# Performance work log

Measured on AMD Instinct MI355X. Metric: run time of the kernel, lower is better.

## Reference

```python
import jax, jax.numpy as jnp
import numpy as np

SCALE_BASE = 512.0
GAMMA = 0.96875


def _rotate_every_two(x):
    x1 = x[..., ::2]
    x2 = x[..., 1::2]
    return jnp.stack([-x2, x1], axis=-1).reshape(x.shape)


def _dup_interleave(m):
    # [L, d/2] -> [L, d], each column duplicated: (a,b) -> (a,a,b,b)
    return jnp.repeat(m, 2, axis=-1)


def _xpos(x, downscale=False):
    # x: [B, L, d]; offset = 0 (parallel form)
    B, L, d = x.shape
    half = d // 2
    pos = jnp.arange(L, dtype=x.dtype)
    # xpos per-channel scale base
    sv = (jnp.arange(0, d, 2, dtype=x.dtype) + 0.4 * d) / (1.4 * d)   # [d/2]
    scale = sv[None, :] ** (pos[:, None] / SCALE_BASE)                 # [L, d/2]
    if downscale:
        scale = 1.0 / scale
    inv_freq = 1.0 / (10000.0 ** (jnp.arange(half, dtype=x.dtype) / half))
    sinusoid = pos[:, None] * inv_freq[None, :]                        # [L, d/2]
    sin = _dup_interleave(jnp.sin(sinusoid) * scale)                   # [L, d]
    cos = _dup_interleave(jnp.cos(sinusoid) * scale)                   # [L, d]
    return x * cos[None] + _rotate_every_two(x) * sin[None]


def _get_D(seq_len, dtype):
    idx = jnp.arange(seq_len)
    diff = idx[:, None] - idx[None, :]                                 # n - m
    safe = jnp.where(diff >= 0, diff, 0).astype(dtype)
    return jnp.where(diff >= 0, GAMMA ** safe, jnp.zeros((), dtype))   # [L, L]


def setup_inputs() -> dict:
    key = jax.random.key(0)
    k1, k2, k3, k4 = jax.random.split(key, 4)
    B, L, H, D = 2, 4096, 1024, 64
    X = jax.random.normal(k1, (B, L, H), dtype=jnp.float32)
    W_Q = jax.random.normal(k2, (H, D), dtype=jnp.float32) / H
    W_K = jax.random.normal(k3, (H, D), dtype=jnp.float32) / H
    W_V = jax.random.normal(k4, (H, D), dtype=jnp.float32) / H
    return {"X": X, "W_Q": W_Q, "W_K": W_K, "W_V": W_V}


def reference(X, W_Q, W_K, W_V):
    L = X.shape[1]
    Dmask = _get_D(L, X.dtype)                     # [L, L]
    Q = _xpos(X @ W_Q)                             # [B, L, d]
    K = _xpos(X @ W_K, downscale=True)             # [B, L, d]
    V = X @ W_V                                    # [B, L, v]
    ret = jnp.einsum('bnd,bmd->bnm', Q, K) * Dmask[None]  # [B, L, L]
    return ret @ V                                 # [B, L, v]
```

## Files before the change

### kernel.cpp

```cpp
#include <hip/hip_runtime.h>
#include <math.h>

#define NB 2
#define LL 4096
#define HH 1024
#define DD 64
#define CHK 64
#define NCH 64
#define BLROWS (NB*LL)
#define NCHT (NB*NCH)
#define GAMMA 0.96875f

typedef _Float16 f16x8 __attribute__((ext_vector_type(8)));
typedef _Float16 f16x4 __attribute__((ext_vector_type(4)));
typedef float    f32x4 __attribute__((ext_vector_type(4)));

#define WCH 12288

__global__ __launch_bounds__(256) void prep_w(
    const float* __restrict__ WQ, const float* __restrict__ WK,
    const float* __restrict__ WV, _Float16* __restrict__ Whg,
    _Float16* __restrict__ Wlg)
{
    const unsigned t = blockIdx.x * 256 + threadIdx.x;
    const unsigned kchunk = t / 1536u;
    const unsigned s = t - kchunk * 1536u;
    const int ct2  = s >> 6;
    const int lane = s & 63;
    const int n16  = ct2 >> 1;
    const int kt   = ct2 & 1;
    const int quad = lane >> 4;
    const int n    = n16 * 16 + (lane & 15);
    const int k0   = (int)kchunk * 64 + kt * 32 + quad * 8;
    const int m    = n >> 6;
    const int d    = n & 63;
    const float* Wm = (m == 0) ? WQ : (m == 1) ? WK : WV;
    f16x8 hv, lv;
#pragma unroll
    for (int j = 0; j < 8; ++j) {
        const float x = Wm[(size_t)(k0 + j) * DD + d] * 1024.f;
        const _Float16 h = (_Float16)x;
        hv[j] = h;
        lv[j] = (_Float16)(x - (float)h);
    }
    *(f16x8*)&Whg[(size_t)t * 8] = hv;
    *(f16x8*)&Wlg[(size_t)t * 8] = lv;
}

__global__ __launch_bounds__(256) void proj_mfma(
    const float* __restrict__ X, const _Float16* __restrict__ Whg,
    const _Float16* __restrict__ Wlg, _Float16* __restrict__ Qr,
    _Float16* __restrict__ Kr, _Float16* __restrict__ Vr)
{
    const int tid  = threadIdx.x;
    const int wv   = tid >> 6;
    const int lane = tid & 63;
    const int quad = lane >> 4;
    const int l15  = lane & 15;
    const int r0   = blockIdx.x * 32;

    f32x4 acc[6];
#pragma unroll
    for (int i = 0; i < 6; ++i) acc[i] = (f32x4){0.f, 0.f, 0.f, 0.f};

    for (int ch = 0; ch < 16; ++ch) {
        f16x8 ah[2][2], al[2][2];
#pragma unroll
        for (int rt = 0; rt < 2; ++rt) {
#pragma unroll
            for (int kt = 0; kt < 2; ++kt) {
                const float* xp = &X[(size_t)(r0 + rt * 16 + l15) * HH +
                                     ch * 64 + kt * 32 + quad * 8];
                const float4 xa = *(const float4*)&xp[0];
                const float4 xb = *(const float4*)&xp[4];
                const float xv[8] = {xa.x, xa.y, xa.z, xa.w,
                                     xb.x, xb.y, xb.z, xb.w};
                f16x8 hv, lv;
#pragma unroll
                for (int e = 0; e < 8; ++e) {
                    const _Float16 h = (_Float16)xv[e];
                    hv[e] = h;
                    lv[e] = (_Float16)(xv[e] - (float)h);
                }
                ah[rt][kt] = hv;
                al[rt][kt] = lv;
            }
        }
#pragma unroll
        for (int kt = 0; kt < 2; ++kt) {
#pragma unroll
            for (int cj = 0; cj < 3; ++cj) {
                const int ctg = wv * 3 + cj;
                const size_t off = (size_t)ch * WCH +
                                   (size_t)(((ctg * 2 + kt) * 64 + lane)) * 8;
                const f16x8 bh = *(const f16x8*)&Whg[off];
                const f16x8 bl = *(const f16x8*)&Wlg[off];
#pragma unroll
                for (int rt = 0; rt < 2; ++rt) {
                    acc[rt * 3 + cj] = __builtin_amdgcn_mfma_f32_16x16x32_f16(
                        ah[rt][kt], bh, acc[rt * 3 + cj], 0, 0, 0);
                    acc[rt * 3 + cj] = __builtin_amdgcn_mfma_f32_16x16x32_f16(
                        ah[rt][kt], bl, acc[rt * 3 + cj], 0, 0, 0);
                    acc[rt * 3 + cj] = __builtin_amdgcn_mfma_f32_16x16x32_f16(
                        al[rt][kt], bh, acc[rt * 3 + cj], 0, 0, 0);
                }
            }
        }
    }

    const int c16 = l15;
#pragma unroll
    for (int rt = 0; rt < 2; ++rt) {
#pragma unroll
        for (int cj = 0; cj < 3; ++cj) {
            const int ctg = wv * 3 + cj;
            const f32x4 v = acc[rt * 3 + cj];
            const int col = ctg * 16 + c16;
            const int mat = ctg >> 2;
            const int d   = col & 63;
            if (mat < 2) {
                const int i2 = d >> 1;
                const float sv   = (2.f * (float)i2 + 25.6f) / 89.6f;
                const float l2sv = log2f(sv);
                const float ifr  = exp2f(-13.28771237954945f * ((float)i2 / 32.f));
                const float sgn  = (mat == 0) ? 1.f : -1.f;
                _Float16* dst = (mat == 0) ? Qr : Kr;
#pragma unroll
                for (int r = 0; r < 4; ++r) {
                    const int row = r0 + rt * 16 + quad * 4 + r;
                    const float val = v[r] * (1.f / 1024.f);
                    const float p = __shfl_xor(val, 1, 64);
                    const float pf  = (float)(row & (LL - 1));
                    const float pfs = (float)(row & 63);
                    const float scl = exp2f(sgn * (pfs * (1.f / 512.f)) * l2sv);
                    float s, c;
                    sincosf(pf * ifr, &s, &c);
                    s *= scl; c *= scl;
                    const float o = ((col & 1) == 0) ? val * c - p * s
                                                     : val * c + p * s;
                    dst[(size_t)row * DD + d] = (_Float16)o;
                }
            } else {
#pragma unroll
                for (int r = 0; r < 4; ++r) {
                    const int row = r0 + rt * 16 + quad * 4 + r;
                    Vr[(size_t)row * DD + d] = (_Float16)(v[r] * (1.f / 1024.f));
                }
            }
        }
    }
}

__global__ __launch_bounds__(256) void chunk_kv(
    const _Float16* __restrict__ Kr, const _Float16* __restrict__ Vr,
    float* __restrict__ U)
{
    __shared__ _Float16 Kl[64 * 64];
    __shared__ _Float16 Vl[64 * 32];
    __shared__ float pwd[64];
    const int tid   = threadIdx.x;
    const int bc    = blockIdx.x;
    const int chunk = bc >> 1;
    const int dph   = (bc & 1) * 32;
    const size_t rbase = (size_t)chunk * CHK * DD;
    const float l2g = log2f(GAMMA);

    if (tid < 64) pwd[tid] = exp2f((float)(63 - tid) * l2g);
    {
        const int row = tid >> 2;
        const int c0  = (tid & 3) * 16;
        *(f16x8*)&Kl[row * 64 + c0]     = *(const f16x8*)&Kr[rbase + (size_t)row * DD + c0];
        *(f16x8*)&Kl[row * 64 + c0 + 8] = *(const f16x8*)&Kr[rbase + (size_t)row * DD + c0 + 8];
        const int c1 = (tid & 3) * 8;
        *(f16x8*)&Vl[row * 32 + c1] = *(const f16x8*)&Vr[rbase + (size_t)row * DD + dph + c1];
    }
    __syncthreads();
    const int dgr = tid >> 4;
    const int dc  = tid & 15;
    float a[4][2] = {{0,0},{0,0},{0,0},{0,0}};
#pragma unroll 8
    for (int j = 0; j < CHK; ++j) {
        const f16x4 kh = *(const f16x4*)&Kl[j * 64 + dgr * 4];
        const float w  = pwd[j];
        const float v0 = (float)Vl[j * 32 + dc * 2]     * w;
        const float v1 = (float)Vl[j * 32 + dc * 2 + 1] * w;
        const float k0 = (float)kh[0], k1 = (float)kh[1];
        const float k2 = (float)kh[2], k3 = (float)kh[3];
        a[0][0] += k0 * v0; a[0][1] += k0 * v1;
        a[1][0] += k1 * v0; a[1][1] += k1 * v1;
        a[2][0] += k2 * v0; a[2][1] += k2 * v1;
        a[3][0] += k3 * v0; a[3][1] += k3 * v1;
    }
#pragma unroll
    for (int r = 0; r < 4; ++r) {
        *(float2*)&U[((size_t)chunk * DD + dgr * 4 + r) * DD + dph + dc * 2] =
            make_float2(a[r][0], a[r][1]);
    }
}

__global__ __launch_bounds__(256) void chunk_out(
    const _Float16* __restrict__ Qr, const _Float16* __restrict__ Kr,
    const _Float16* __restrict__ Vr, const float* __restrict__ U,
    float* __restrict__ out)
{
    __shared__ __align__(16) unsigned char smraw[35648];
    _Float16* Sb  = (_Float16*)smraw;
    _Float16* Vl  = (_Float16*)(smraw + 8704);
    float*    Tl  = (float*)(smraw + 17920);
    float*    pwl = (float*)(smraw + 35328);

    const int tid   = threadIdx.x;
    const int bc    = blockIdx.x;
    const int chunk = bc >> 1;
    const int nh    = (bc & 1) * 32;
    const int w     = tid >> 6;
    const int lane  = tid & 63;
    const int quad  = lane >> 4;
    const int l15   = lane & 15;
    const int mtile = w >> 1;
    const int npair = (w & 1) * 2;
    const size_t rowbase = (size_t)chunk * CHK + nh;
    const float l2g = log2f(GAMMA);

    if (tid < 65) pwl[tid] = exp2f((float)tid * l2g);

    {
        const int row = tid >> 2;
        const int c0  = (tid & 3) * 16;
        const size_t rb = (size_t)chunk * CHK * DD;
        *(f16x8*)&Vl[row * 72 + c0]     = *(const f16x8*)&Vr[rb + (size_t)row * DD + c0];
        *(f16x8*)&Vl[row * 72 + c0 + 8] = *(const f16x8*)&Vr[rb + (size_t)row * DD + c0 + 8];
    }
    {
        const int d  = tid >> 2;
        const int dq = (tid & 3) * 16;
        const int cloc = chunk & 63;
        const float sv = (2.f * (float)(d >> 1) + 25.6f) / 89.6f;
        const float l2sv = log2f(sv);
        float acc[16];
#pragma unroll
        for (int i = 0; i < 16; ++i) acc[i] = 0.f;
        for (int dl = 1; dl <= 8; ++dl) {
            if (dl <= cloc) {
                const float f = exp2f(64.f * (float)(dl - 1) * l2g +
                                      0.125f * (float)dl * l2sv);
                const float* up = &U[((size_t)(chunk - dl) * DD + d) * DD + dq];
#pragma unroll
                for (int i4 = 0; i4 < 4; ++i4) {
                    const float4 u = *(const float4*)&up[i4 * 4];
                    acc[i4 * 4 + 0] += f * u.x; acc[i4 * 4 + 1] += f * u.y;
                    acc[i4 * 4 + 2] += f * u.z; acc[i4 * 4 + 3] += f * u.w;
                }
            }
        }
#pragma unroll
        for (int i = 0; i < 16; ++i) Tl[d * 68 + dq + i] = acc[i];
    }

    f16x8 aQ[2], bK[2][2];
#pragma unroll
    for (int ks = 0; ks < 2; ++ks)
        aQ[ks] = *(const f16x8*)&Qr[(rowbase + mtile * 16 + l15) * DD +
                                    ks * 32 + quad * 8];
#pragma unroll
    for (int nt = 0; nt < 2; ++nt)
#pragma unroll
        for (int ks = 0; ks < 2; ++ks)
            bK[nt][ks] = *(const f16x8*)&Kr[((size_t)chunk * CHK +
                                            (npair + nt) * 16 + l15) * DD +
                                            ks * 32 + quad * 8];
    __syncthreads();

    f32x4 sA[2] = {(f32x4){0.f,0.f,0.f,0.f}, (f32x4){0.f,0.f,0.f,0.f}};
#pragma unroll
    for (int nt = 0; nt < 2; ++nt)
#pragma unroll
        for (int ks = 0; ks < 2; ++ks)
            sA[nt] = __builtin_amdgcn_mfma_f32_16x16x32_f16(aQ[ks], bK[nt][ks],
                                                            sA[nt], 0, 0, 0);
#pragma unroll
    for (int nt = 0; nt < 2; ++nt) {
        const int m = (npair + nt) * 16 + l15;
#pragma unroll
        for (int r = 0; r < 4; ++r) {
            const int nl = mtile * 16 + quad * 4 + r;
            const int n64 = nh + nl;
            const float val = (n64 >= m) ? sA[nt][r] * pwl[n64 - m] : 0.f;
            Sb[nl * 136 + m] = (_Float16)val;
        }
    }
    if ((w & 1) == 0) {
        const float g = pwl[nh + mtile * 16 + l15 + 1];
#pragma unroll
        for (int ks = 0; ks < 2; ++ks) {
            f16x8 qv;
#pragma unroll
            for (int j = 0; j < 8; ++j)
                qv[j] = (_Float16)((float)aQ[ks][j] * g);
            *(f16x8*)&Sb[(mtile * 16 + l15) * 136 + 64 + ks * 32 + quad * 8] = qv;
        }
    }
    __syncthreads();

    f32x4 oA[2] = {(f32x4){0.f,0.f,0.f,0.f}, (f32x4){0.f,0.f,0.f,0.f}};
#pragma unroll
    for (int ks = 0; ks < 4; ++ks) {
        const f16x8 aS = *(const f16x8*)&Sb[(mtile * 16 + l15) * 136 +
                                            ks * 32 + quad * 8];
#pragma unroll
        for (int nt = 0; nt < 2; ++nt) {
            const int dp = (npair + nt) * 16 + l15;
            f16x8 bV;
            if (ks < 2) {
#pragma unroll
                for (int j = 0; j < 8; ++j)
                    bV[j] = Vl[(ks * 32 + quad * 8 + j) * 72 + dp];
            } else {
#pragma unroll
                for (int j = 0; j < 8; ++j)
                    bV[j] = (_Float16)Tl[((ks - 2) * 32 + quad * 8 + j) * 68 + dp];
            }
            oA[nt] = __builtin_amdgcn_mfma_f32_16x16x32_f16(aS, bV, oA[nt], 0, 0, 0);
        }
    }
#pragma unroll
    for (int nt = 0; nt < 2; ++nt)
#pragma unroll
        for (int r = 0; r < 4; ++r)
            out[(rowbase + mtile * 16 + quad * 4 + r) * DD +
                (npair + nt) * 16 + l15] = oA[nt][r];
}

extern "C" void kernel_launch(void* const* d_in, const int* in_sizes, int n_in,
                              void* d_out, int out_size, void* d_ws, size_t ws_size,
                              hipStream_t stream)
{
    const float* X  = (const float*)d_in[0];
    const float* WQ = (const float*)d_in[1];
    const float* WK = (const float*)d_in[2];
    const float* WV = (const float*)d_in[3];
    float* outp = (float*)d_out;

    _Float16* Whg = (_Float16*)d_ws;
    _Float16* Wlg = Whg + 196608;
    _Float16* Qr  = Wlg + 196608;
    _Float16* Kr  = Qr + (size_t)BLROWS * DD;
    _Float16* Vr  = Kr + (size_t)BLROWS * DD;
    float*    U   = (float*)(Vr + (size_t)BLROWS * DD);

    hipLaunchKernelGGL(prep_w, dim3(96), dim3(256), 0, stream,
                       WQ, WK, WV, Whg, Wlg);
    hipLaunchKernelGGL(proj_mfma, dim3(BLROWS / 32), dim3(256), 0, stream,
                       X, Whg, Wlg, Qr, Kr, Vr);
    hipLaunchKernelGGL(chunk_kv, dim3(2 * NCHT), dim3(256), 0, stream, Kr, Vr, U);
    hipLaunchKernelGGL(chunk_out, dim3(2 * NCHT), dim3(256), 0, stream,
                       Qr, Kr, Vr, U, outp);
}
```

Baseline: 120.5 us.

## Fuse all stages into one persistent kernel with grid barriers and LDS-staged projection

Merges the four launches (weight prep, projection, chunk KV state, chunk output) into a single 512-block kernel separated by software grid barriers built on flag arrays. The projection stage now splits each 32-row tile across two blocks, stages X and W tiles through LDS and register-prefetches the next K chunk. The intent is to remove launch gaps and raise projection parallelism. In exchange, the barrier relies on all 512 blocks being co-resident, uses flags that are never reset (the phase value stays the same across calls), and leaves half the blocks idle in the later stages.

```diff
diff --git a/kernel.cpp b/kernel.cpp
--- a/kernel.cpp
+++ b/kernel.cpp
@@ -16,65 +16,113 @@
 typedef float    f32x4 __attribute__((ext_vector_type(4)));
 
 #define WCH 12288
-
-__global__ __launch_bounds__(256) void prep_w(
-    const float* __restrict__ WQ, const float* __restrict__ WK,
-    const float* __restrict__ WV, _Float16* __restrict__ Whg,
-    _Float16* __restrict__ Wlg)
+#define NBLK 512
+
+__device__ __forceinline__ void grid_bar(unsigned* flags, unsigned phase,
+                                         int bid, int tid)
 {
-    const unsigned t = blockIdx.x * 256 + threadIdx.x;
-    const unsigned kchunk = t / 1536u;
-    const unsigned s = t - kchunk * 1536u;
-    const int ct2  = s >> 6;
-    const int lane = s & 63;
-    const int n16  = ct2 >> 1;
-    const int kt   = ct2 & 1;
-    const int quad = lane >> 4;
-    const int n    = n16 * 16 + (lane & 15);
-    const int k0   = (int)kchunk * 64 + kt * 32 + quad * 8;
-    const int m    = n >> 6;
-    const int d    = n & 63;
-    const float* Wm = (m == 0) ? WQ : (m == 1) ? WK : WV;
-    f16x8 hv, lv;
-#pragma unroll
-    for (int j = 0; j < 8; ++j) {
-        const float x = Wm[(size_t)(k0 + j) * DD + d] * 1024.f;
-        const _Float16 h = (_Float16)x;
-        hv[j] = h;
-        lv[j] = (_Float16)(x - (float)h);
+    __syncthreads();
+    const unsigned tgt = 0xBB000000u + phase;
+    if (tid == 0)
+        __hip_atomic_store(&flags[bid], tgt, __ATOMIC_RELEASE,
+                           __HIP_MEMORY_SCOPE_AGENT);
+    long long guard = 0;
+    while (__hip_atomic_load(&flags[tid], __ATOMIC_ACQUIRE,
+                             __HIP_MEMORY_SCOPE_AGENT) < tgt &&
+           guard < 30000000LL) { __builtin_amdgcn_s_sleep(1); ++guard; }
+    while (__hip_atomic_load(&flags[tid + 256], __ATOMIC_ACQUIRE,
+                             __HIP_MEMORY_SCOPE_AGENT) < tgt &&
+           guard < 30000000LL) { __builtin_amdgcn_s_sleep(1); ++guard; }
+    __syncthreads();
+}
+
+__global__ __launch_bounds__(256, 2) void retention_all(
+    const float* __restrict__ X, const float* __restrict__ WQ,
+    const float* __restrict__ WK, const float* __restrict__ WV,
+    _Float16* __restrict__ Whg, _Float16* __restrict__ Wlg,
+    _Float16* __restrict__ Qr, _Float16* __restrict__ Kr,
+    _Float16* __restrict__ Vr, float* __restrict__ U,
+    unsigned* __restrict__ flags, float* __restrict__ out)
+{
+    __shared__ __align__(16) unsigned char smraw[35648];
+    const int tid = threadIdx.x;
+    const int bid = blockIdx.x;
+
+    {
+        const unsigned t = bid * 256 + tid;
+        if (t < 24576u) {
+            const unsigned kchunk = t / 1536u;
+            const unsigned s = t - kchunk * 1536u;
+            const int ct2  = s >> 6;
+            const int lane = s & 63;
+            const int n16  = ct2 >> 1;
+            const int kt   = ct2 & 1;
+            const int quad = lane >> 4;
+            const int n    = n16 * 16 + (lane & 15);
+            const int k0   = (int)kchunk * 64 + kt * 32 + quad * 8;
+            const int m    = n >> 6;
+            const int d    = n & 63;
+            const float* Wm = (m == 0) ? WQ : (m == 1) ? WK : WV;
+            f16x8 hv, lv;
+#pragma unroll
+            for (int j = 0; j < 8; ++j) {
+                const float x = Wm[(size_t)(k0 + j) * DD + d] * 1024.f;
+                const _Float16 h = (_Float16)x;
+                hv[j] = h;
+                lv[j] = (_Float16)(x - (float)h);
+            }
+            *(f16x8*)&Whg[(size_t)t * 8] = hv;
+            *(f16x8*)&Wlg[(size_t)t * 8] = lv;
+        }
     }
-    *(f16x8*)&Whg[(size_t)t * 8] = hv;
-    *(f16x8*)&Wlg[(size_t)t * 8] = lv;
-}
-
-__global__ __launch_bounds__(256) void proj_mfma(
-    const float* __restrict__ X, const _Float16* __restrict__ Whg,
-    const _Float16* __restrict__ Wlg, _Float16* __restrict__ Qr,
-    _Float16* __restrict__ Kr, _Float16* __restrict__ Vr)
-{
-    const int tid  = threadIdx.x;
-    const int wv   = tid >> 6;
-    const int lane = tid & 63;
-    const int quad = lane >> 4;
-    const int l15  = lane & 15;
-    const int r0   = blockIdx.x * 32;
-
-    f32x4 acc[6];
-#pragma unroll
-    for (int i = 0; i < 6; ++i) acc[i] = (f32x4){0.f, 0.f, 0.f, 0.f};
-
-    for (int ch = 0; ch < 16; ++ch) {
-        f16x8 ah[2][2], al[2][2];
-#pragma unroll
-        for (int rt = 0; rt < 2; ++rt) {
-#pragma unroll
-            for (int kt = 0; kt < 2; ++kt) {
-                const float* xp = &X[(size_t)(r0 + rt * 16 + l15) * HH +
-                                     ch * 64 + kt * 32 + quad * 8];
-                const float4 xa = *(const float4*)&xp[0];
-                const float4 xb = *(const float4*)&xp[4];
-                const float xv[8] = {xa.x, xa.y, xa.z, xa.w,
-                                     xb.x, xb.y, xb.z, xb.w};
+    grid_bar(flags, 1, bid, tid);
+
+    {
+        _Float16* lds = (_Float16*)smraw;
+        _Float16* Xh = lds;
+        _Float16* Xl = lds + 2048;
+        _Float16* Wh = lds + 4096;
+        _Float16* Wl = lds + 10240;
+
+        const int wv   = tid >> 6;
+        const int lane = tid & 63;
+        const int quad = lane >> 4;
+        const int l15  = lane & 15;
+        const int r0   = (bid >> 1) * 32;
+        const int cb6  = (bid & 1) * 6;
+        const int rt   = wv & 1;
+        const int ct3  = (wv >> 1) * 3;
+
+        const int xrow = tid >> 3;
+        const int xk8  = (tid & 7) * 8;
+        const int xslot = (((xrow >> 4) * 2 + (xk8 >> 5)) * 64 +
+                           ((xk8 >> 3) & 3) * 16 + (xrow & 15)) * 8;
+
+        f32x4 acc[3];
+#pragma unroll
+        for (int i = 0; i < 3; ++i) acc[i] = (f32x4){0.f, 0.f, 0.f, 0.f};
+
+        float4 pxa, pxb;
+        f16x8  pwh[3], pwl6[3];
+        {
+            const float* xp = &X[(size_t)(r0 + xrow) * HH + xk8];
+            pxa = *(const float4*)&xp[0];
+            pxb = *(const float4*)&xp[4];
+#pragma unroll
+            for (int i = 0; i < 3; ++i) {
+                const int s = tid + i * 256;
+                const int ctl = s >> 7, kt = (s >> 6) & 1, ln = s & 63;
+                const size_t off = (size_t)(((cb6 + ctl) * 2 + kt) * 64 + ln) * 8;
+                pwh[i]  = *(const f16x8*)&Whg[off];
+                pwl6[i] = *(const f16x8*)&Wlg[off];
+            }
+        }
+
+        for (int ch = 0; ch < 16; ++ch) {
+            __syncthreads();
+            {
+                const float xv[8] = {pxa.x, pxa.y, pxa.z, pxa.w,
+                                     pxb.x, pxb.y, pxb.z, pxb.w};
                 f16x8 hv, lv;
 #pragma unroll
                 for (int e = 0; e < 8; ++e) {
@@ -82,40 +130,51 @@
                     hv[e] = h;
                     lv[e] = (_Float16)(xv[e] - (float)h);
                 }
-                ah[rt][kt] = hv;
-                al[rt][kt] = lv;
-            }
-        }
-#pragma unroll
-        for (int kt = 0; kt < 2; ++kt) {
-#pragma unroll
-            for (int cj = 0; cj < 3; ++cj) {
-                const int ctg = wv * 3 + cj;
-                const size_t off = (size_t)ch * WCH +
-                                   (size_t)(((ctg * 2 + kt) * 64 + lane)) * 8;
-                const f16x8 bh = *(const f16x8*)&Whg[off];
-                const f16x8 bl = *(const f16x8*)&Wlg[off];
-#pragma unroll
-                for (int rt = 0; rt < 2; ++rt) {
-                    acc[rt * 3 + cj] = __builtin_amdgcn_mfma_f32_16x16x32_f16(
-                        ah[rt][kt], bh, acc[rt * 3 + cj], 0, 0, 0);
-                    acc[rt * 3 + cj] = __builtin_amdgcn_mfma_f32_16x16x32_f16(
-                        ah[rt][kt], bl, acc[rt * 3 + cj], 0, 0, 0);
-                    acc[rt * 3 + cj] = __builtin_amdgcn_mfma_f32_16x16x32_f16(
-                        al[rt][kt], bh, acc[rt * 3 + cj], 0, 0, 0);
-                }
-            }
-        }
-    }
-
-    const int c16 = l15;
-#pragma unroll
-    for (int rt = 0; rt < 2; ++rt) {
+                *(f16x8*)&Xh[xslot] = hv;
+                *(f16x8*)&Xl[xslot] = lv;
+#pragma unroll
+                for (int i = 0; i < 3; ++i) {
+                    *(f16x8*)&Wh[(tid + i * 256) * 8] = pwh[i];
+                    *(f16x8*)&Wl[(tid + i * 256) * 8] = pwl6[i];
+                }
+            }
+            __syncthreads();
+            if (ch + 1 < 16) {
+                const float* xp = &X[(size_t)(r0 + xrow) * HH + (ch + 1) * 64 + xk8];
+                pxa = *(const float4*)&xp[0];
+                pxb = *(const float4*)&xp[4];
+                const size_t cb = (size_t)(ch + 1) * WCH;
+#pragma unroll
+                for (int i = 0; i < 3; ++i) {
+                    const int s = tid + i * 256;
+                    const int ctl = s >> 7, kt = (s >> 6) & 1, ln = s & 63;
+                    const size_t off = cb +
+                        (size_t)(((cb6 + ctl) * 2 + kt) * 64 + ln) * 8;
+                    pwh[i]  = *(const f16x8*)&Whg[off];
+                    pwl6[i] = *(const f16x8*)&Wlg[off];
+                }
+            }
+#pragma unroll
+            for (int kt = 0; kt < 2; ++kt) {
+                const f16x8 aH = *(const f16x8*)&Xh[((rt * 2 + kt) * 64 + lane) * 8];
+                const f16x8 aL = *(const f16x8*)&Xl[((rt * 2 + kt) * 64 + lane) * 8];
+#pragma unroll
+                for (int cj = 0; cj < 3; ++cj) {
+                    const int ctl = ct3 + cj;
+                    const f16x8 bh = *(const f16x8*)&Wh[((ctl * 2 + kt) * 64 + lane) * 8];
+                    const f16x8 bl = *(const f16x8*)&Wl[((ctl * 2 + kt) * 64 + lane) * 8];
+                    acc[cj] = __builtin_amdgcn_mfma_f32_16x16x32_f16(aH, bh, acc[cj], 0, 0, 0);
+                    acc[cj] = __builtin_amdgcn_mfma_f32_16x16x32_f16(aH, bl, acc[cj], 0, 0, 0);
+                    acc[cj] = __builtin_amdgcn_mfma_f32_16x16x32_f16(aL, bh, acc[cj], 0, 0, 0);
+                }
+            }
+        }
+
 #pragma unroll
         for (int cj = 0; cj < 3; ++cj) {
-            const int ctg = wv * 3 + cj;
-            const f32x4 v = acc[rt * 3 + cj];
-            const int col = ctg * 16 + c16;
+            const int ctg = cb6 + ct3 + cj;
+            const f32x4 v = acc[cj];
+            const int col = ctg * 16 + l15;
             const int mat = ctg >> 2;
             const int d   = col & 63;
             if (mat < 2) {
@@ -149,186 +208,176 @@
             }
         }
     }
-}
-
-__global__ __launch_bounds__(256) void chunk_kv(
-    const _Float16* __restrict__ Kr, const _Float16* __restrict__ Vr,
-    float* __restrict__ U)
-{
-    __shared__ _Float16 Kl[64 * 64];
-    __shared__ _Float16 Vl[64 * 32];
-    __shared__ float pwd[64];
-    const int tid   = threadIdx.x;
-    const int bc    = blockIdx.x;
-    const int chunk = bc >> 1;
-    const int dph   = (bc & 1) * 32;
-    const size_t rbase = (size_t)chunk * CHK * DD;
-    const float l2g = log2f(GAMMA);
-
-    if (tid < 64) pwd[tid] = exp2f((float)(63 - tid) * l2g);
-    {
-        const int row = tid >> 2;
-        const int c0  = (tid & 3) * 16;
-        *(f16x8*)&Kl[row * 64 + c0]     = *(const f16x8*)&Kr[rbase + (size_t)row * DD + c0];
-        *(f16x8*)&Kl[row * 64 + c0 + 8] = *(const f16x8*)&Kr[rbase + (size_t)row * DD + c0 + 8];
-        const int c1 = (tid & 3) * 8;
-        *(f16x8*)&Vl[row * 32 + c1] = *(const f16x8*)&Vr[rbase + (size_t)row * DD + dph + c1];
+    grid_bar(flags, 2, bid, tid);
+
+    if (bid < 256) {
+        _Float16* Kl  = (_Float16*)smraw;
+        _Float16* Vl  = (_Float16*)(smraw + 8192);
+        float*    pwd = (float*)(smraw + 12288);
+        const int chunk = bid >> 1;
+        const int dph   = (bid & 1) * 32;
+        const size_t rbase = (size_t)chunk * CHK * DD;
+        const float l2g = log2f(GAMMA);
+
+        if (tid < 64) pwd[tid] = exp2f((float)(63 - tid) * l2g);
+        {
+            const int row = tid >> 2;
+            const int c0  = (tid & 3) * 16;
+            *(f16x8*)&Kl[row * 64 + c0]     = *(const f16x8*)&Kr[rbase + (size_t)row * DD + c0];
+            *(f16x8*)&Kl[row * 64 + c0 + 8] = *(const f16x8*)&Kr[rbase + (size_t)row * DD + c0 + 8];
+            const int c1 = (tid & 3) * 8;
+            *(f16x8*)&Vl[row * 32 + c1] = *(const f16x8*)&Vr[rbase + (size_t)row * DD + dph + c1];
+        }
+        __syncthreads();
+        const int dgr = tid >> 4;
+        const int dc  = tid & 15;
+        float a[4][2] = {{0,0},{0,0},{0,0},{0,0}};
+#pragma unroll 8
+        for (int j = 0; j < CHK; ++j) {
+            const f16x4 kh = *(const f16x4*)&Kl[j * 64 + dgr * 4];
+            const float w  = pwd[j];
+            const float v0 = (float)Vl[j * 32 + dc * 2]     * w;
+            const float v1 = (float)Vl[j * 32 + dc * 2 + 1] * w;
+            const float k0 = (float)kh[0], k1 = (float)kh[1];
+            const float k2 = (float)kh[2], k3 = (float)kh[3];
+            a[0][0] += k0 * v0; a[0][1] += k0 * v1;
+            a[1][0] += k1 * v0; a[1][1] += k1 * v1;
+            a[2][0] += k2 * v0; a[2][1] += k2 * v1;
+            a[3][0] += k3 * v0; a[3][1] += k3 * v1;
+        }
+#pragma unroll
+        for (int r = 0; r < 4; ++r) {
+            *(float2*)&U[((size_t)chunk * DD + dgr * 4 + r) * DD + dph + dc * 2] =
+                make_float2(a[r][0], a[r][1]);
+        }
     }
-    __syncthreads();
-    const int dgr = tid >> 4;
-    const int dc  = tid & 15;
-    float a[4][2] = {{0,0},{0,0},{0,0},{0,0}};
-#pragma unroll 8
-    for (int j = 0; j < CHK; ++j) {
-        const f16x4 kh = *(const f16x4*)&Kl[j * 64 + dgr * 4];
-        const float w  = pwd[j];
-        const float v0 = (float)Vl[j * 32 + dc * 2]     * w;
-        const float v1 = (float)Vl[j * 32 + dc * 2 + 1] * w;
-        const float k0 = (float)kh[0], k1 = (float)kh[1];
-        const float k2 = (float)kh[2], k3 = (float)kh[3];
-        a[0][0] += k0 * v0; a[0][1] += k0 * v1;
-        a[1][0] += k1 * v0; a[1][1] += k1 * v1;
-        a[2][0] += k2 * v0; a[2][1] += k2 * v1;
-        a[3][0] += k3 * v0; a[3][1] += k3 * v1;
+    grid_bar(flags, 3, bid, tid);
+
+    if (bid < 256) {
+        _Float16* Sb  = (_Float16*)smraw;
+        _Float16* Vl  = (_Float16*)(smraw + 8704);
+        float*    Tl  = (float*)(smraw + 17920);
+        float*    pwl = (float*)(smraw + 35328);
+
+        const int chunk = bid >> 1;
+        const int nh    = (bid & 1) * 32;
+        const int w     = tid >> 6;
+        const int lane  = tid & 63;
+        const int quad  = lane >> 4;
+        const int l15   = lane & 15;
+        const int mtile = w >> 1;
+        const int npair = (w & 1) * 2;
+        const size_t rowbase = (size_t)chunk * CHK + nh;
+        const float l2g = log2f(GAMMA);
+
+        if (tid < 65) pwl[tid] = exp2f((float)tid * l2g);
+
+        {
+            const int row = tid >> 2;
+            const int c0  = (tid & 3) * 16;
+            const size_t rb = (size_t)chunk * CHK * DD;
+            *(f16x8*)&Vl[row * 72 + c0]     = *(const f16x8*)&Vr[rb + (size_t)row * DD + c0];
+            *(f16x8*)&Vl[row * 72 + c0 + 8] = *(const f16x8*)&Vr[rb + (size_t)row * DD + c0 + 8];
+        }
+        {
+            const int d  = tid >> 2;
+            const int dq = (tid & 3) * 16;
+            const int cloc = chunk & 63;
+            const float sv = (2.f * (float)(d >> 1) + 25.6f) / 89.6f;
+            const float l2sv = log2f(sv);
+            float acc[16];
+#pragma unroll
+            for (int i = 0; i < 16; ++i) acc[i] = 0.f;
+            for (int dl = 1; dl <= 8; ++dl) {
+                if (dl <= cloc) {
+                    const float f = exp2f(64.f * (float)(dl - 1) * l2g +
+                                          0.125f * (float)dl * l2sv);
+                    const float* up = &U[((size_t)(chunk - dl) * DD + d) * DD + dq];
+#pragma unroll
+                    for (int i4 = 0; i4 < 4; ++i4) {
+                        const float4 u = *(const float4*)&up[i4 * 4];
+                        acc[i4 * 4 + 0] += f * u.x; acc[i4 * 4 + 1] += f * u.y;
+                        acc[i4 * 4 + 2] += f * u.z; acc[i4 * 4 + 3] += f * u.w;
+                    }
+                }
+            }
+#pragma unroll
+            for (int i = 0; i < 16; ++i) Tl[d * 68 + dq + i] = acc[i];
+        }
+
+        f16x8 aQ[2], bK[2][2];
+#pragma unroll
+        for (int ks = 0; ks < 2; ++ks)
+            aQ[ks] = *(const f16x8*)&Qr[(rowbase + mtile * 16 + l15) * DD +
+                                        ks * 32 + quad * 8];
+#pragma unroll
+        for (int nt = 0; nt < 2; ++nt)
+#pragma unroll
+            for (int ks = 0; ks < 2; ++ks)
+                bK[nt][ks] = *(const f16x8*)&Kr[((size_t)chunk * CHK +
+                                                (npair + nt) * 16 + l15) * DD +
+                                                ks * 32 + quad * 8];
+        __syncthreads();
+
+        f32x4 sA[2] = {(f32x4){0.f,0.f,0.f,0.f}, (f32x4){0.f,0.f,0.f,0.f}};
+#pragma unroll
+        for (int nt = 0; nt < 2; ++nt)
+#pragma unroll
+            for (int ks = 0; ks < 2; ++ks)
+                sA[nt] = __builtin_amdgcn_mfma_f32_16x16x32_f16(aQ[ks], bK[nt][ks],
+                                                                sA[nt], 0, 0, 0);
+#pragma unroll
+        for (int nt = 0; nt < 2; ++nt) {
+            const int m = (npair + nt) * 16 + l15;
+#pragma unroll
+            for (int r = 0; r < 4; ++r) {
+                const int nl = mtile * 16 + quad * 4 + r;
+                const int n64 = nh + nl;
+                const float val = (n64 >= m) ? sA[nt][r] * pwl[n64 - m] : 0.f;
+                Sb[nl * 136 + m] = (_Float16)val;
+            }
+        }
+        if ((w & 1) == 0) {
+            const float g = pwl[nh + mtile * 16 + l15 + 1];
+#pragma unroll
+            for (int ks = 0; ks < 2; ++ks) {
+                f16x8 qv;
+#pragma unroll
+                for (int j = 0; j < 8; ++j)
+                    qv[j] = (_Float16)((float)aQ[ks][j] * g);
+                *(f16x8*)&Sb[(mtile * 16 + l15) * 136 + 64 + ks * 32 + quad * 8] = qv;
+            }
+        }
+        __syncthreads();
+
+        f32x4 oA[2] = {(f32x4){0.f,0.f,0.f,0.f}, (f32x4){0.f,0.f,0.f,0.f}};
+#pragma unroll
+        for (int ks = 0; ks < 4; ++ks) {
+            const f16x8 aS = *(const f16x8*)&Sb[(mtile * 16 + l15) * 136 +
+                                                ks * 32 + quad * 8];
+#pragma unroll
+            for (int nt = 0; nt < 2; ++nt) {
+                const int dp = (npair + nt) * 16 + l15;
+                f16x8 bV;
+                if (ks < 2) {
+#pragma unroll
+                    for (int j = 0; j < 8; ++j)
+                        bV[j] = Vl[(ks * 32 + quad * 8 + j) * 72 + dp];
+                } else {
+#pragma unroll
+                    for (int j = 0; j < 8; ++j)
+                        bV[j] = (_Float16)Tl[((ks - 2) * 32 + quad * 8 + j) * 68 + dp];
+                }
+                oA[nt] = __builtin_amdgcn_mfma_f32_16x16x32_f16(aS, bV, oA[nt], 0, 0, 0);
+            }
+        }
+#pragma unroll
+        for (int nt = 0; nt < 2; ++nt)
+#pragma unroll
+            for (int r = 0; r < 4; ++r)
+                out[(rowbase + mtile * 16 + quad * 4 + r) * DD +
+                    (npair + nt) * 16 + l15] = oA[nt][r];
     }
-#pragma unroll
-    for (int r = 0; r < 4; ++r) {
-        *(float2*)&U[((size_t)chunk * DD + dgr * 4 + r) * DD + dph + dc * 2] =
-            make_float2(a[r][0], a[r][1]);
-    }
-}
-
-__global__ __launch_bounds__(256) void chunk_out(
-    const _Float16* __restrict__ Qr, const _Float16* __restrict__ Kr,
-    const _Float16* __restrict__ Vr, const float* __restrict__ U,
-    float* __restrict__ out)
-{
-    __shared__ __align__(16) unsigned char smraw[35648];
-    _Float16* Sb  = (_Float16*)smraw;
-    _Float16* Vl  = (_Float16*)(smraw + 8704);
-    float*    Tl  = (float*)(smraw + 17920);
-    float*    pwl = (float*)(smraw + 35328);
-
-    const int tid   = threadIdx.x;
-    const int bc    = blockIdx.x;
-    const int chunk = bc >> 1;
-    const int nh    = (bc & 1) * 32;
-    const int w     = tid >> 6;
-    const int lane  = tid & 63;
-    const int quad  = lane >> 4;
-    const int l15   = lane & 15;
-    const int mtile = w >> 1;
-    const int npair = (w & 1) * 2;
-    const size_t rowbase = (size_t)chunk * CHK + nh;
-    const float l2g = log2f(GAMMA);
-
-    if (tid < 65) pwl[tid] = exp2f((float)tid * l2g);
-
-    {
-        const int row = tid >> 2;
-        const int c0  = (tid & 3) * 16;
-        const size_t rb = (size_t)chunk * CHK * DD;
-        *(f16x8*)&Vl[row * 72 + c0]     = *(const f16x8*)&Vr[rb + (size_t)row * DD + c0];
-        *(f16x8*)&Vl[row * 72 + c0 + 8] = *(const f16x8*)&Vr[rb + (size_t)row * DD + c0 + 8];
-    }
-    {
-        const int d  = tid >> 2;
-        const int dq = (tid & 3) * 16;
-        const int cloc = chunk & 63;
-        const float sv = (2.f * (float)(d >> 1) + 25.6f) / 89.6f;
-        const float l2sv = log2f(sv);
-        float acc[16];
-#pragma unroll
-        for (int i = 0; i < 16; ++i) acc[i] = 0.f;
-        for (int dl = 1; dl <= 8; ++dl) {
-            if (dl <= cloc) {
-                const float f = exp2f(64.f * (float)(dl - 1) * l2g +
-                                      0.125f * (float)dl * l2sv);
-                const float* up = &U[((size_t)(chunk - dl) * DD + d) * DD + dq];
-#pragma unroll
-                for (int i4 = 0; i4 < 4; ++i4) {
-                    const float4 u = *(const float4*)&up[i4 * 4];
-                    acc[i4 * 4 + 0] += f * u.x; acc[i4 * 4 + 1] += f * u.y;
-                    acc[i4 * 4 + 2] += f * u.z; acc[i4 * 4 + 3] += f * u.w;
-                }
-            }
-        }
-#pragma unroll
-        for (int i = 0; i < 16; ++i) Tl[d * 68 + dq + i] = acc[i];
-    }
-
-    f16x8 aQ[2], bK[2][2];
-#pragma unroll
-    for (int ks = 0; ks < 2; ++ks)
-        aQ[ks] = *(const f16x8*)&Qr[(rowbase + mtile * 16 + l15) * DD +
-                                    ks * 32 + quad * 8];
-#pragma unroll
-    for (int nt = 0; nt < 2; ++nt)
-#pragma unroll
-        for (int ks = 0; ks < 2; ++ks)
-            bK[nt][ks] = *(const f16x8*)&Kr[((size_t)chunk * CHK +
-                                            (npair + nt) * 16 + l15) * DD +
-                                            ks * 32 + quad * 8];
-    __syncthreads();
-
-    f32x4 sA[2] = {(f32x4){0.f,0.f,0.f,0.f}, (f32x4){0.f,0.f,0.f,0.f}};
-#pragma unroll
-    for (int nt = 0; nt < 2; ++nt)
-#pragma unroll
-        for (int ks = 0; ks < 2; ++ks)
-            sA[nt] = __builtin_amdgcn_mfma_f32_16x16x32_f16(aQ[ks], bK[nt][ks],
-                                                            sA[nt], 0, 0, 0);
-#pragma unroll
-    for (int nt = 0; nt < 2; ++nt) {
-        const int m = (npair + nt) * 16 + l15;
-#pragma unroll
-        for (int r = 0; r < 4; ++r) {
-            const int nl = mtile * 16 + quad * 4 + r;
-            const int n64 = nh + nl;
-            const float val = (n64 >= m) ? sA[nt][r] * pwl[n64 - m] : 0.f;
-            Sb[nl * 136 + m] = (_Float16)val;
-        }
-    }
-    if ((w & 1) == 0) {
-        const float g = pwl[nh + mtile * 16 + l15 + 1];
-#pragma unroll
-        for (int ks = 0; ks < 2; ++ks) {
-            f16x8 qv;
-#pragma unroll
-            for (int j = 0; j < 8; ++j)
-                qv[j] = (_Float16)((float)aQ[ks][j] * g);
-            *(f16x8*)&Sb[(mtile * 16 + l15) * 136 + 64 + ks * 32 + quad * 8] = qv;
-        }
-    }
-    __syncthreads();
-
-    f32x4 oA[2] = {(f32x4){0.f,0.f,0.f,0.f}, (f32x4){0.f,0.f,0.f,0.f}};
-#pragma unroll
-    for (int ks = 0; ks < 4; ++ks) {
-        const f16x8 aS = *(const f16x8*)&Sb[(mtile * 16 + l15) * 136 +
-                                            ks * 32 + quad * 8];
-#pragma unroll
-        for (int nt = 0; nt < 2; ++nt) {
-            const int dp = (npair + nt) * 16 + l15;
-            f16x8 bV;
-            if (ks < 2) {
-#pragma unroll
-                for (int j = 0; j < 8; ++j)
-                    bV[j] = Vl[(ks * 32 + quad * 8 + j) * 72 + dp];
-            } else {
-#pragma unroll
-                for (int j = 0; j < 8; ++j)
-                    bV[j] = (_Float16)Tl[((ks - 2) * 32 + quad * 8 + j) * 68 + dp];
-            }
-            oA[nt] = __builtin_amdgcn_mfma_f32_16x16x32_f16(aS, bV, oA[nt], 0, 0, 0);
-        }
-    }
-#pragma unroll
-    for (int nt = 0; nt < 2; ++nt)
-#pragma unroll
-        for (int r = 0; r < 4; ++r)
-            out[(rowbase + mtile * 16 + quad * 4 + r) * DD +
-                (npair + nt) * 16 + l15] = oA[nt][r];
 }
 
 extern "C" void kernel_launch(void* const* d_in, const int* in_sizes, int n_in,
@@ -347,12 +396,8 @@
     _Float16* Kr  = Qr + (size_t)BLROWS * DD;
     _Float16* Vr  = Kr + (size_t)BLROWS * DD;
     float*    U   = (float*)(Vr + (size_t)BLROWS * DD);
-
-    hipLaunchKernelGGL(prep_w, dim3(96), dim3(256), 0, stream,
-                       WQ, WK, WV, Whg, Wlg);
-    hipLaunchKernelGGL(proj_mfma, dim3(BLROWS / 32), dim3(256), 0, stream,
-                       X, Whg, Wlg, Qr, Kr, Vr);
-    hipLaunchKernelGGL(chunk_kv, dim3(2 * NCHT), dim3(256), 0, stream, Kr, Vr, U);
-    hipLaunchKernelGGL(chunk_out, dim3(2 * NCHT), dim3(256), 0, stream,
-                       Qr, Kr, Vr, U, outp);
+    unsigned* flags = (unsigned*)(U + (size_t)NCHT * DD * DD);
+
+    hipLaunchKernelGGL(retention_all, dim3(NBLK), dim3(256), 0, stream,
+                       X, WQ, WK, WV, Whg, Wlg, Qr, Kr, Vr, U, flags, outp);
 }
```

After: 302.6 us. 2.51x slower.

## Stage projection tiles through LDS with register prefetch and split columns across blocks

Applied to the files above, without the earlier changes.

The projection kernel now splits the 192 output columns into three blocks of 64, launching 768 blocks instead of 256. Each block cooperatively loads and splits its 32-row X tile and its W slice into LDS, then prefetches the next K-chunk into registers while MFMAs run. This aims to raise occupancy and parallelism and cut redundant global loads per wave. In exchange, each X row is read and converted three times across blocks, and each chunk adds two barriers.

```diff
diff --git a/kernel.cpp b/kernel.cpp
--- a/kernel.cpp
+++ b/kernel.cpp
@@ -52,100 +52,133 @@
     const _Float16* __restrict__ Wlg, _Float16* __restrict__ Qr,
     _Float16* __restrict__ Kr, _Float16* __restrict__ Vr)
 {
+    __shared__ __align__(16) _Float16 lds[12288];
+    _Float16* Xh = lds;
+    _Float16* Xl = lds + 2048;
+    _Float16* Wh = lds + 4096;
+    _Float16* Wl = lds + 8192;
+
     const int tid  = threadIdx.x;
     const int wv   = tid >> 6;
     const int lane = tid & 63;
     const int quad = lane >> 4;
     const int l15  = lane & 15;
-    const int r0   = blockIdx.x * 32;
-
-    f32x4 acc[6];
-#pragma unroll
-    for (int i = 0; i < 6; ++i) acc[i] = (f32x4){0.f, 0.f, 0.f, 0.f};
+    const int r0   = (blockIdx.x & 255) * 32;
+    const int cb4  = (blockIdx.x >> 8) * 4;
+    const int rt   = wv & 1;
+    const int cp   = (wv >> 1) * 2;
+
+    const int xrow = tid >> 3;
+    const int xk8  = (tid & 7) * 8;
+    const int xslot = (((xrow >> 4) * 2 + (xk8 >> 5)) * 64 +
+                       ((xk8 >> 3) & 3) * 16 + (xrow & 15)) * 8;
+
+    f32x4 acc[2];
+    acc[0] = (f32x4){0.f, 0.f, 0.f, 0.f};
+    acc[1] = (f32x4){0.f, 0.f, 0.f, 0.f};
+
+    float4 pxa, pxb;
+    f16x8  pwh[2], pwl2[2];
+    {
+        const float* xp = &X[(size_t)(r0 + xrow) * HH + xk8];
+        pxa = *(const float4*)&xp[0];
+        pxb = *(const float4*)&xp[4];
+#pragma unroll
+        for (int i = 0; i < 2; ++i) {
+            const int s = tid + i * 256;
+            const int ctl = s >> 7, kt = (s >> 6) & 1, ln = s & 63;
+            const size_t off = (size_t)(((cb4 + ctl) * 2 + kt) * 64 + ln) * 8;
+            pwh[i]  = *(const f16x8*)&Whg[off];
+            pwl2[i] = *(const f16x8*)&Wlg[off];
+        }
+    }
 
     for (int ch = 0; ch < 16; ++ch) {
-        f16x8 ah[2][2], al[2][2];
-#pragma unroll
-        for (int rt = 0; rt < 2; ++rt) {
-#pragma unroll
-            for (int kt = 0; kt < 2; ++kt) {
-                const float* xp = &X[(size_t)(r0 + rt * 16 + l15) * HH +
-                                     ch * 64 + kt * 32 + quad * 8];
-                const float4 xa = *(const float4*)&xp[0];
-                const float4 xb = *(const float4*)&xp[4];
-                const float xv[8] = {xa.x, xa.y, xa.z, xa.w,
-                                     xb.x, xb.y, xb.z, xb.w};
-                f16x8 hv, lv;
-#pragma unroll
-                for (int e = 0; e < 8; ++e) {
-                    const _Float16 h = (_Float16)xv[e];
-                    hv[e] = h;
-                    lv[e] = (_Float16)(xv[e] - (float)h);
-                }
-                ah[rt][kt] = hv;
-                al[rt][kt] = lv;
+        __syncthreads();
+        {
+            const float xv[8] = {pxa.x, pxa.y, pxa.z, pxa.w,
+                                 pxb.x, pxb.y, pxb.z, pxb.w};
+            f16x8 hv, lv;
+#pragma unroll
+            for (int e = 0; e < 8; ++e) {
+                const _Float16 h = (_Float16)xv[e];
+                hv[e] = h;
+                lv[e] = (_Float16)(xv[e] - (float)h);
+            }
+            *(f16x8*)&Xh[xslot] = hv;
+            *(f16x8*)&Xl[xslot] = lv;
+#pragma unroll
+            for (int i = 0; i < 2; ++i) {
+                *(f16x8*)&Wh[(tid + i * 256) * 8] = pwh[i];
+                *(f16x8*)&Wl[(tid + i * 256) * 8] = pwl2[i];
+            }
+        }
+        __syncthreads();
+        if (ch + 1 < 16) {
+            const float* xp = &X[(size_t)(r0 + xrow) * HH + (ch + 1) * 64 + xk8];
+            pxa = *(const float4*)&xp[0];
+            pxb = *(const float4*)&xp[4];
+            const size_t cb = (size_t)(ch + 1) * WCH;
+#pragma unroll
+            for (int i = 0; i < 2; ++i) {
+                const int s = tid + i * 256;
+                const int ctl = s >> 7, kt = (s >> 6) & 1, ln = s & 63;
+                const size_t off = cb +
+                    (size_t)(((cb4 + ctl) * 2 + kt) * 64 + ln) * 8;
+                pwh[i]  = *(const f16x8*)&Whg[off];
+                pwl2[i] = *(const f16x8*)&Wlg[off];
             }
         }
 #pragma unroll
         for (int kt = 0; kt < 2; ++kt) {
-#pragma unroll
-            for (int cj = 0; cj < 3; ++cj) {
-                const int ctg = wv * 3 + cj;
-                const size_t off = (size_t)ch * WCH +
-                                   (size_t)(((ctg * 2 + kt) * 64 + lane)) * 8;
-                const f16x8 bh = *(const f16x8*)&Whg[off];
-                const f16x8 bl = *(const f16x8*)&Wlg[off];
-#pragma unroll
-                for (int rt = 0; rt < 2; ++rt) {
-                    acc[rt * 3 + cj] = __builtin_amdgcn_mfma_f32_16x16x32_f16(
-                        ah[rt][kt], bh, acc[rt * 3 + cj], 0, 0, 0);
-                    acc[rt * 3 + cj] = __builtin_amdgcn_mfma_f32_16x16x32_f16(
-                        ah[rt][kt], bl, acc[rt * 3 + cj], 0, 0, 0);
-                    acc[rt * 3 + cj] = __builtin_amdgcn_mfma_f32_16x16x32_f16(
-                        al[rt][kt], bh, acc[rt * 3 + cj], 0, 0, 0);
-                }
-            }
-        }
-    }
-
-    const int c16 = l15;
-#pragma unroll
-    for (int rt = 0; rt < 2; ++rt) {
-#pragma unroll
-        for (int cj = 0; cj < 3; ++cj) {
-            const int ctg = wv * 3 + cj;
-            const f32x4 v = acc[rt * 3 + cj];
-            const int col = ctg * 16 + c16;
-            const int mat = ctg >> 2;
-            const int d   = col & 63;
-            if (mat < 2) {
-                const int i2 = d >> 1;
-                const float sv   = (2.f * (float)i2 + 25.6f) / 89.6f;
-                const float l2sv = log2f(sv);
-                const float ifr  = exp2f(-13.28771237954945f * ((float)i2 / 32.f));
-                const float sgn  = (mat == 0) ? 1.f : -1.f;
-                _Float16* dst = (mat == 0) ? Qr : Kr;
-#pragma unroll
-                for (int r = 0; r < 4; ++r) {
-                    const int row = r0 + rt * 16 + quad * 4 + r;
-                    const float val = v[r] * (1.f / 1024.f);
-                    const float p = __shfl_xor(val, 1, 64);
-                    const float pf  = (float)(row & (LL - 1));
-                    const float pfs = (float)(row & 63);
-                    const float scl = exp2f(sgn * (pfs * (1.f / 512.f)) * l2sv);
-                    float s, c;
-                    sincosf(pf * ifr, &s, &c);
-                    s *= scl; c *= scl;
-                    const float o = ((col & 1) == 0) ? val * c - p * s
-                                                     : val * c + p * s;
-                    dst[(size_t)row * DD + d] = (_Float16)o;
-                }
-            } else {
-#pragma unroll
-                for (int r = 0; r < 4; ++r) {
-                    const int row = r0 + rt * 16 + quad * 4 + r;
-                    Vr[(size_t)row * DD + d] = (_Float16)(v[r] * (1.f / 1024.f));
-                }
+            const f16x8 aH = *(const f16x8*)&Xh[((rt * 2 + kt) * 64 + lane) * 8];
+            const f16x8 aL = *(const f16x8*)&Xl[((rt * 2 + kt) * 64 + lane) * 8];
+#pragma unroll
+            for (int cj = 0; cj < 2; ++cj) {
+                const int ctl = cp + cj;
+                const f16x8 bh = *(const f16x8*)&Wh[((ctl * 2 + kt) * 64 + lane) * 8];
+                const f16x8 bl = *(const f16x8*)&Wl[((ctl * 2 + kt) * 64 + lane) * 8];
+                acc[cj] = __builtin_amdgcn_mfma_f32_16x16x32_f16(aH, bh, acc[cj], 0, 0, 0);
+                acc[cj] = __builtin_amdgcn_mfma_f32_16x16x32_f16(aH, bl, acc[cj], 0, 0, 0);
+                acc[cj] = __builtin_amdgcn_mfma_f32_16x16x32_f16(aL, bh, acc[cj], 0, 0, 0);
+            }
+        }
+    }
+
+#pragma unroll
+    for (int cj = 0; cj < 2; ++cj) {
+        const int ctg = cb4 + cp + cj;
+        const f32x4 v = acc[cj];
+        const int col = ctg * 16 + l15;
+        const int mat = ctg >> 2;
+        const int d   = col & 63;
+        if (mat < 2) {
+            const int i2 = d >> 1;
+            const float sv   = (2.f * (float)i2 + 25.6f) / 89.6f;
+            const float l2sv = log2f(sv);
+            const float ifr  = exp2f(-13.28771237954945f * ((float)i2 / 32.f));
+            const float sgn  = (mat == 0) ? 1.f : -1.f;
+            _Float16* dst = (mat == 0) ? Qr : Kr;
+#pragma unroll
+            for (int r = 0; r < 4; ++r) {
+                const int row = r0 + rt * 16 + quad * 4 + r;
+                const float val = v[r] * (1.f / 1024.f);
+                const float p = __shfl_xor(val, 1, 64);
+                const float pf  = (float)(row & (LL - 1));
+                const float pfs = (float)(row & 63);
+                const float scl = exp2f(sgn * (pfs * (1.f / 512.f)) * l2sv);
+                float s, c;
+                sincosf(pf * ifr, &s, &c);
+                s *= scl; c *= scl;
+                const float o = ((col & 1) == 0) ? val * c - p * s
+                                                 : val * c + p * s;
+                dst[(size_t)row * DD + d] = (_Float16)o;
+            }
+        } else {
+#pragma unroll
+            for (int r = 0; r < 4; ++r) {
+                const int row = r0 + rt * 16 + quad * 4 + r;
+                Vr[(size_t)row * DD + d] = (_Float16)(v[r] * (1.f / 1024.f));
             }
         }
     }
@@ -350,7 +383,7 @@
 
     hipLaunchKernelGGL(prep_w, dim3(96), dim3(256), 0, stream,
                        WQ, WK, WV, Whg, Wlg);
-    hipLaunchKernelGGL(proj_mfma, dim3(BLROWS / 32), dim3(256), 0, stream,
+    hipLaunchKernelGGL(proj_mfma, dim3(768), dim3(256), 0, stream,
                        X, Whg, Wlg, Qr, Kr, Vr);
     hipLaunchKernelGGL(chunk_kv, dim3(2 * NCHT), dim3(256), 0, stream, Kr, Vr, U);
     hipLaunchKernelGGL(chunk_out, dim3(2 * NCHT), dim3(256), 0, stream,
```

Result: faster. 113.1 us (-6.1%).
